# Performance work log

Measured on AMD Instinct MI355X. Metric: run time of the kernel, lower is better.

The kernel has to match this reference:

```python
import jax, jax.numpy as jnp
import numpy as np

B = 32768
H = 320          # pred_hidden
V = 34           # num_classes
BLANK = V - 1    # padding_idx for embedding


def setup_inputs() -> dict:
    key = jax.random.key(0)
    ks = jax.random.split(key, 12)
    s = 0.05
    embed_W = jax.random.normal(ks[0], (V, H), jnp.float32) * s
    embed_W = embed_W.at[BLANK].set(0.0)  # padding_idx row is zeros in torch
    return {
        "x": jax.random.randint(ks[1], (B,), 0, V, jnp.int32),
        "enc_proj_line": jax.random.normal(ks[2], (B, H), jnp.float32),
        "h": jax.random.normal(ks[3], (1, B, H), jnp.float32),
        "c": jax.random.normal(ks[4], (1, B, H), jnp.float32),
        "embed_W": embed_W,
        "W_ih": jax.random.normal(ks[5], (4 * H, H), jnp.float32) * s,
        "W_hh": jax.random.normal(ks[6], (4 * H, H), jnp.float32) * s,
        "b_ih": jax.random.normal(ks[7], (4 * H,), jnp.float32) * s,
        "b_hh": jax.random.normal(ks[8], (4 * H,), jnp.float32) * s,
        "pred_W": jax.random.normal(ks[9], (H, H), jnp.float32) * s,
        "pred_b": jnp.zeros((H,), jnp.float32),
        "joint_W": jax.random.normal(ks[10], (V, H), jnp.float32) * s,
        "joint_b": jnp.zeros((V,), jnp.float32),
    }


def reference(x, enc_proj_line, h, c, embed_W, W_ih, W_hh, b_ih, b_hh,
              pred_W, pred_b, joint_W, joint_b):
    # embedding lookup: [B, H]
    emb = embed_W[x]
    # single-timestep LSTM cell (torch gate order: i, f, g, o)
    gates = emb @ W_ih.T + b_ih + h[0] @ W_hh.T + b_hh  # [B, 4H]
    i, f, g, o = jnp.split(gates, 4, axis=-1)
    i = jax.nn.sigmoid(i)
    f = jax.nn.sigmoid(f)
    g = jnp.tanh(g)
    o = jax.nn.sigmoid(o)
    c_new = f * c[0] + i * g                 # [B, H]
    h_new = o * jnp.tanh(c_new)              # [B, H] == g[0] (lstm output)
    # pred projection + joint
    pred_proj = h_new @ pred_W.T + pred_b    # [B, H]
    joint_out = (enc_proj_line + pred_proj) @ joint_W.T + joint_b  # [B, V]
    dec = jnp.argmax(joint_out, axis=-1)
    return dec, h_new[None], c_new[None]
```

## Files before the change

### kernel.cpp

```cpp
#include <hip/hip_runtime.h>
#include <math.h>

#define NB 32768
#define H 320
#define V 34
#define N4 1280
#define BM 128
#define BN 128
#define BK 32
#define KSTEPS (H / BK)
#define NWG ((NB / BM) * (N4 / BN))

typedef _Float16 f16;
typedef f16 f16x4 __attribute__((ext_vector_type(4)));
typedef f16 f16x8 __attribute__((ext_vector_type(8)));
typedef float f32x4 __attribute__((ext_vector_type(4)));

#define WS_GTP 0
#define WS_JB2 54400
#define WS_B_BYTE 217744
#define BT_COUNT (N4 * H)
#define WS_JP_BYTE 1856144
#define JP_COUNT (48 * 640)
#define WS_AT_BYTE 1979136
#define AT_COUNT (NB * H)

#define JBM 64
#define JBK 32
#define JKSTEPS 20

#define PREP_P4 1280
#define PREP_P2 50
#define PREP_P0 170
#define PREP_P3 120
#define PREP_NWG (PREP_P4 + PREP_P2 + PREP_P0 + PREP_P3 + 1)

__device__ __forceinline__ float sigf(float x) {
    return 1.0f / (1.0f + __expf(-x));
}
__device__ __forceinline__ float tanh_fast(float x) {
    return 1.0f - 2.0f / (1.0f + __expf(2.0f * x));
}

typedef const __attribute__((address_space(1))) unsigned int* gas_t;
typedef __attribute__((address_space(3))) unsigned int* las_t;

__device__ __forceinline__ void split8(const float* e, f16x8& p1, f16x8& p2) {
    #pragma unroll
    for (int j = 0; j < 8; ++j) {
        f16 a = (f16)e[j];
        p1[j] = a;
        p2[j] = (f16)((e[j] - (float)a) * 2048.0f);
    }
}

__global__ void prep(const float* __restrict__ embed_W,
                     const float* __restrict__ W_ih,
                     const float* __restrict__ b_ih,
                     const float* __restrict__ b_hh,
                     const float* __restrict__ pred_W,
                     const float* __restrict__ pred_b,
                     const float* __restrict__ joint_W,
                     const float* __restrict__ joint_b,
                     const float* __restrict__ W_hh,
                     const float* __restrict__ h_in,
                     float* __restrict__ ws) {
    const int bid = blockIdx.x;
    const int t = threadIdx.x;
    if (bid < PREP_P4) {
        int id = bid * 256 + t;
        int ks = id >> 15, m = id & 32767;
        const float* src = h_in + (size_t)m * H + ks * 32;
        f16* at1 = (f16*)((char*)ws + WS_AT_BYTE);
        f16* at2 = at1 + AT_COUNT;
        size_t tbase = ((size_t)(m >> 7) * KSTEPS + ks) * 4096
                       + ((m & 127) >> 4) * 512 + (m & 15) * 8;
        #pragma unroll
        for (int g = 0; g < 4; ++g) {
            float4 v0 = *(const float4*)(src + g * 8);
            float4 v1 = *(const float4*)(src + g * 8 + 4);
            float e[8] = {v0.x, v0.y, v0.z, v0.w, v1.x, v1.y, v1.z, v1.w};
            f16x8 p1, p2;
            split8(e, p1, p2);
            *(f16x8*)(at1 + tbase + g * 128) = p1;
            *(f16x8*)(at2 + tbase + g * 128) = p2;
        }
    } else if (bid < PREP_P4 + PREP_P2) {
        int id = (bid - PREP_P4) * 256 + t;
        int ks = id / 1280, n = id - ks * 1280;
        int orig = (n & 3) * H + (n >> 2);
        const float* src = W_hh + (size_t)orig * H + ks * 32;
        f16* bt1 = (f16*)((char*)ws + WS_B_BYTE);
        f16* bt2 = bt1 + BT_COUNT;
        size_t tbase = ((size_t)(n >> 7) * KSTEPS + ks) * 4096
                       + ((n & 127) >> 4) * 512 + (n & 15) * 8;
        #pragma unroll
        for (int g = 0; g < 4; ++g) {
            float4 v0 = *(const float4*)(src + g * 8);
            float4 v1 = *(const float4*)(src + g * 8 + 4);
            float e[8] = {v0.x, v0.y, v0.z, v0.w, v1.x, v1.y, v1.z, v1.w};
            f16x8 p1, p2;
            split8(e, p1, p2);
            *(f16x8*)(bt1 + tbase + g * 128) = p1;
            *(f16x8*)(bt2 + tbase + g * 128) = p2;
        }
    } else if (bid < PREP_P4 + PREP_P2 + PREP_P0) {
        int id = (bid - PREP_P4 - PREP_P2) * 256 + t;
        int v = id / N4, n = id % N4;
        int orig = (n & 3) * H + (n >> 2);
        float acc = b_ih[orig] + b_hh[orig];
        const float* e = embed_W + (size_t)v * H;
        const float* w = W_ih + (size_t)orig * H;
        for (int k = 0; k < H; k += 4) {
            float4 e4 = *(const float4*)(e + k);
            float4 w4 = *(const float4*)(w + k);
            acc = fmaf(e4.x, w4.x, acc);
            acc = fmaf(e4.y, w4.y, acc);
            acc = fmaf(e4.z, w4.z, acc);
            acc = fmaf(e4.w, w4.w, acc);
        }
        ws[WS_GTP + id] = acc;
    } else if (bid < PREP_P4 + PREP_P2 + PREP_P0 + PREP_P3) {
        int id = (bid - PREP_P4 - PREP_P2 - PREP_P0) * 256 + t;
        int n = id / 640, k = id % 640;
        float wv = 0.0f;
        if (n < V) {
            if (k < H) {
                wv = joint_W[(size_t)n * H + k];
            } else {
                float acc = 0.0f;
                const float* jw = joint_W + (size_t)n * H;
                for (int j = 0; j < H; ++j)
                    acc = fmaf(jw[j], pred_W[(size_t)j * H + (k - H)], acc);
                wv = acc;
            }
        }
        f16 w1 = (f16)wv;
        f16 w2 = (f16)((wv - (float)w1) * 2048.0f);
        int kk = k & 31;
        int off = (k >> 5) * 1536 + (n >> 4) * 512 + (kk >> 3) * 128
                  + (n & 15) * 8 + (kk & 7);
        f16* jp1 = (f16*)((char*)ws + WS_JP_BYTE);
        jp1[off] = w1;
        jp1[JP_COUNT + off] = w2;
    } else {
        if (t < V) {
            float acc = joint_b[t];
            const float* jw = joint_W + (size_t)t * H;
            for (int j = 0; j < H; ++j)
                acc = fmaf(jw[j], pred_b[j], acc);
            ws[WS_JB2 + t] = acc;
        }
    }
}

__launch_bounds__(256, 2)
__global__ void lstm_gemm_fast(const int* __restrict__ x,
                               const float* __restrict__ c_in,
                               const float* __restrict__ ws,
                               float* __restrict__ out) {
    __shared__ __align__(16) char smem[65536];
    const int tid = threadIdx.x, lane = tid & 63, w = tid >> 6;

    int l = (blockIdx.x & 7) * (NWG / 8) + (blockIdx.x >> 3);
    const int mb = l / (N4 / BN);
    const int nb = l % (N4 / BN);
    const int m0 = mb * BM, n0 = nb * BN;

    const f16* At1 = (const f16*)((const char*)ws + WS_AT_BYTE);
    const f16* At2 = At1 + AT_COUNT;
    const f16* Bt1 = (const f16*)((const char*)ws + WS_B_BYTE);
    const f16* Bt2 = Bt1 + BT_COUNT;
    const float* gtp = ws + WS_GTP;
    float* hn_out = out + NB;
    float* cn_out = out + NB + (size_t)NB * H;

    const int asub = (w >> 1) * 4;
    const int bsub = (w & 1) * 4;
    const int lo = lane * 8;

    auto stageB = [&](int ks, int parity) {
        const f16* srcp = (w < 2) ? Bt1 : Bt2;
        const f16* src = srcp + (size_t)(nb * KSTEPS + ks) * 4096 + (w & 1) * 2048;
        char* dst = smem + parity * 16384 + (w >> 1) * 8192 + (w & 1) * 4096;
        #pragma unroll
        for (int i = 0; i < 4; ++i) {
            __builtin_amdgcn_global_load_lds(
                (gas_t)(const void*)(src + i * 512 + lane * 8),
                (las_t)(void*)(dst + i * 1024), 16, 0, 0);
        }
    };

    f32x4 accM[4][4], accC[4][4];
    #pragma unroll
    for (int i = 0; i < 4; ++i)
        #pragma unroll
        for (int j = 0; j < 4; ++j) {
            accM[i][j] = (f32x4){0.f, 0.f, 0.f, 0.f};
            accC[i][j] = (f32x4){0.f, 0.f, 0.f, 0.f};
        }

    f16x8 a1r[2][4], a2r[4], b1[4], b2[4];

    stageB(0, 0);
    __builtin_amdgcn_sched_barrier(0);
    {
        const f16* a1b = At1 + (size_t)(mb * KSTEPS + 0) * 4096;
        #pragma unroll
        for (int mi = 0; mi < 4; ++mi)
            a1r[0][mi] = *(const f16x8*)(a1b + (asub + mi) * 512 + lo);
    }
    asm volatile("s_waitcnt vmcnt(4)" ::: "memory");
    __builtin_amdgcn_sched_barrier(0);
    __builtin_amdgcn_s_barrier();

    #pragma unroll
    for (int t = 0; t < KSTEPS; ++t) {
        const int cb = t & 1;
        {
            const f16* a2b = At2 + (size_t)(mb * KSTEPS + t) * 4096;
            #pragma unroll
            for (int mi = 0; mi < 4; ++mi)
                a2r[mi] = *(const f16x8*)(a2b + (asub + mi) * 512 + lo);
        }
        __builtin_amdgcn_sched_barrier(0);
        if (t < KSTEPS - 1) {
            stageB(t + 1, cb ^ 1);
            __builtin_amdgcn_sched_barrier(0);
            const f16* a1b = At1 + (size_t)(mb * KSTEPS + (t + 1)) * 4096;
            #pragma unroll
            for (int mi = 0; mi < 4; ++mi)
                a1r[cb ^ 1][mi] = *(const f16x8*)(a1b + (asub + mi) * 512 + lo);
            __builtin_amdgcn_sched_barrier(0);
        }

        const f16* B1 = (const f16*)(smem + cb * 16384);
        const f16* B2 = B1 + 4096;

        #pragma unroll
        for (int nj = 0; nj < 4; ++nj)
            b1[nj] = *(const f16x8*)(B1 + (bsub + nj) * 512 + lo);
        __builtin_amdgcn_s_setprio(1);
        #pragma unroll
        for (int mi = 0; mi < 4; ++mi)
            #pragma unroll
            for (int nj = 0; nj < 4; ++nj)
                accM[mi][nj] = __builtin_amdgcn_mfma_f32_16x16x32_f16(
                    a1r[cb][mi], b1[nj], accM[mi][nj], 0, 0, 0);
        __builtin_amdgcn_s_setprio(0);
        #pragma unroll
        for (int nj = 0; nj < 4; ++nj)
            b2[nj] = *(const f16x8*)(B2 + (bsub + nj) * 512 + lo);
        __builtin_amdgcn_s_setprio(1);
        #pragma unroll
        for (int mi = 0; mi < 4; ++mi)
            #pragma unroll
            for (int nj = 0; nj < 4; ++nj)
                accC[mi][nj] = __builtin_amdgcn_mfma_f32_16x16x32_f16(
                    a1r[cb][mi], b2[nj], accC[mi][nj], 0, 0, 0);
        #pragma unroll
        for (int mi = 0; mi < 4; ++mi)
            #pragma unroll
            for (int nj = 0; nj < 4; ++nj)
                accC[mi][nj] = __builtin_amdgcn_mfma_f32_16x16x32_f16(
                    a2r[mi], b1[nj], accC[mi][nj], 0, 0, 0);
        __builtin_amdgcn_s_setprio(0);

        if (t < KSTEPS - 1) {
            asm volatile("s_waitcnt vmcnt(4)" ::: "memory");
            __builtin_amdgcn_sched_barrier(0);
            __builtin_amdgcn_s_barrier();
        } else {
            __syncthreads();
        }
    }

    const int wm = (w >> 1) * 64, wn = (w & 1) * 64;
    float* gates = (float*)smem;
    #pragma unroll
    for (int mi = 0; mi < 4; ++mi)
        #pragma unroll
        for (int nj = 0; nj < 4; ++nj) {
            f32x4 vm = accM[mi][nj];
            f32x4 vc = accC[mi][nj];
            int n = wn + nj * 16 + (lane & 15);
            int mb4 = wm + mi * 16 + (lane >> 4) * 4;
            #pragma unroll
            for (int q = 0; q < 4; ++q) {
                int row = mb4 + q;
                gates[row * 128 + (n ^ ((row & 7) << 2))] =
                    fmaf(vc[q], 1.0f / 2048.0f, vm[q]);
            }
        }
    __syncthreads();

    const int hk0 = n0 >> 2;
    #pragma unroll 4
    for (int it = 0; it < 16; ++it) {
        int idx = it * 256 + tid;
        int ml = idx >> 5, hkl = idx & 31;
        int k0 = (ml & 7) << 2;
        f32x4 g4 = *(const f32x4*)&gates[ml * 128 + ((hkl * 4) ^ k0)];
        int m = m0 + ml;
        int hk = hk0 + hkl;
        int xv = x[m];
        float4 b4 = *(const float4*)(gtp + (size_t)xv * N4 + n0 + hkl * 4);
        float ig = sigf(g4[0] + b4.x);
        float fg = sigf(g4[1] + b4.y);
        float gg = tanh_fast(g4[2] + b4.z);
        float og = sigf(g4[3] + b4.w);
        float cv = c_in[(size_t)m * H + hk];
        float cn = fmaf(fg, cv, ig * gg);
        float hn = og * tanh_fast(cn);
        hn_out[(size_t)m * H + hk] = hn;
        cn_out[(size_t)m * H + hk] = cn;
    }
}

__launch_bounds__(256, 2)
__global__ void joint_argmax(const float* __restrict__ enc,
                             const float* __restrict__ ws,
                             float* __restrict__ out) {
    __shared__ __align__(16) char smem[28672];
    const int tid = threadIdx.x, lane = tid & 63, w = tid >> 6;
    const int m0 = blockIdx.x * JBM;

    const f16* Jp1 = (const f16*)((const char*)ws + WS_JP_BYTE);
    const f16* Jp2 = Jp1 + JP_COUNT;
    const float* hn = out + NB;
    const float* jb2 = ws + WS_JB2;

    f16* base = (f16*)smem;

    f32x4 accM[3], accC[3];
    #pragma unroll
    for (int j = 0; j < 3; ++j) {
        accM[j] = (f32x4){0.f, 0.f, 0.f, 0.f};
        accC[j] = (f32x4){0.f, 0.f, 0.f, 0.f};
    }

    auto stage = [&](int t, f16* A1, f16* A2, f16* B1, f16* B2) {
        const float* srcp = (t < 10) ? enc : hn;
        const int koff = (t % 10) * JBK;
        int row = (tid >> 6) * 16 + (tid & 15);
        int k0 = ((tid & 63) >> 4) * 8;
        const float* sp = srcp + (size_t)(m0 + row) * H + koff + k0;
        float4 v0 = *(const float4*)sp;
        float4 v1 = *(const float4*)(sp + 4);
        float e[8] = {v0.x, v0.y, v0.z, v0.w, v1.x, v1.y, v1.z, v1.w};
        f16x8 p1, p2;
        split8(e, p1, p2);
        *(f16x8*)(A1 + tid * 8) = p1;
        *(f16x8*)(A2 + tid * 8) = p2;
        if (tid < 192) {
            *(int4*)(B1 + tid * 8) = *(const int4*)(Jp1 + t * 1536 + tid * 8);
            *(int4*)(B2 + tid * 8) = *(const int4*)(Jp2 + t * 1536 + tid * 8);
        }
    };

    stage(0, base, base + 2048, base + 4096, base + 5632);
    __syncthreads();

    const int lo = lane * 8;
    int cur = 0;
    for (int t = 0; t < JKSTEPS; ++t) {
        if (t < JKSTEPS - 1) {
            f16* nb_ = base + (cur ^ 1) * 7168;
            stage(t + 1, nb_, nb_ + 2048, nb_ + 4096, nb_ + 5632);
        }
        f16* A1 = base + cur * 7168;
        f16* A2 = A1 + 2048;
        f16* B1 = A1 + 4096;
        f16* B2 = A1 + 5632;

        f16x8 a1 = *(const f16x8*)(A1 + w * 512 + lo);
        f16x8 a2 = *(const f16x8*)(A2 + w * 512 + lo);
        f16x8 b1[3], b2[3];
        #pragma unroll
        for (int nj = 0; nj < 3; ++nj) {
            b1[nj] = *(const f16x8*)(B1 + nj * 512 + lo);
            b2[nj] = *(const f16x8*)(B2 + nj * 512 + lo);
        }
        #pragma unroll
        for (int nj = 0; nj < 3; ++nj) {
            accM[nj] = __builtin_amdgcn_mfma_f32_16x16x32_f16(a1, b1[nj], accM[nj], 0, 0, 0);
            accC[nj] = __builtin_amdgcn_mfma_f32_16x16x32_f16(a1, b2[nj], accC[nj], 0, 0, 0);
            accC[nj] = __builtin_amdgcn_mfma_f32_16x16x32_f16(a2, b1[nj], accC[nj], 0, 0, 0);
        }
        __syncthreads();
        cur ^= 1;
    }

    float* lg = (float*)smem;
    const int wm = w * 16;
    #pragma unroll
    for (int nj = 0; nj < 3; ++nj) {
        int n = nj * 16 + (lane & 15);
        int mr = wm + (lane >> 4) * 4;
        #pragma unroll
        for (int q = 0; q < 4; ++q)
            lg[(mr + q) * 49 + n] = fmaf(accC[nj][q], 1.0f / 2048.0f, accM[nj][q]);
    }
    __syncthreads();

    if (tid < JBM) {
        const float* row = lg + tid * 49;
        float best = row[0] + jb2[0];
        int bi = 0;
        #pragma unroll
        for (int v = 1; v < V; ++v) {
            float t2 = row[v] + jb2[v];
            if (t2 > best) { best = t2; bi = v; }
        }
        out[m0 + tid] = (float)bi;
    }
}

extern "C" void kernel_launch(void* const* d_in, const int* in_sizes, int n_in,
                              void* d_out, int out_size, void* d_ws, size_t ws_size,
                              hipStream_t stream) {
    const int*   x       = (const int*)  d_in[0];
    const float* enc     = (const float*)d_in[1];
    const float* h       = (const float*)d_in[2];
    const float* c       = (const float*)d_in[3];
    const float* embed_W = (const float*)d_in[4];
    const float* W_ih    = (const float*)d_in[5];
    const float* W_hh    = (const float*)d_in[6];
    const float* b_ih    = (const float*)d_in[7];
    const float* b_hh    = (const float*)d_in[8];
    const float* pred_W  = (const float*)d_in[9];
    const float* pred_b  = (const float*)d_in[10];
    const float* joint_W = (const float*)d_in[11];
    const float* joint_b = (const float*)d_in[12];
    float* out = (float*)d_out;
    float* ws  = (float*)d_ws;

    prep<<<PREP_NWG, 256, 0, stream>>>(embed_W, W_ih, b_ih, b_hh,
                                       pred_W, pred_b, joint_W, joint_b,
                                       W_hh, h, ws);
    lstm_gemm_fast<<<NWG, 256, 0, stream>>>(x, c, ws, out);
    joint_argmax<<<NB / JBM, 256, 0, stream>>>(enc, ws, out);
}
```

Baseline: 162.5 us.

## Merge split-precision accumulators and halve LDS to raise GEMM occupancy

Drops the separate correction accumulator by folding the fp16 residual terms into the main accumulator. The A-residual is stored unscaled, and the high A part is multiplied by 2^-11 in registers before it meets the scaled B residual. The gate epilogue now runs in two halves so it fits in 32 KB of shared memory, and launch bounds go from 2 to 3 blocks per CU. The aim is fewer VGPRs and less LDS so more waves can hide latency. The costs are extra fp16 multiplies, an extra barrier round in the epilogue, and possible precision loss from small unscaled residuals underflowing in fp16.

```diff
diff --git a/kernel.cpp b/kernel.cpp
--- a/kernel.cpp
+++ b/kernel.cpp
@@ -51,6 +51,15 @@
         f16 a = (f16)e[j];
         p1[j] = a;
         p2[j] = (f16)((e[j] - (float)a) * 2048.0f);
+    }
+}
+
+__device__ __forceinline__ void split8_res(const float* e, f16x8& p1, f16x8& p2) {
+    #pragma unroll
+    for (int j = 0; j < 8; ++j) {
+        f16 a = (f16)e[j];
+        p1[j] = a;
+        p2[j] = (f16)(e[j] - (float)a);
     }
 }
 
@@ -81,7 +90,7 @@
             float4 v1 = *(const float4*)(src + g * 8 + 4);
             float e[8] = {v0.x, v0.y, v0.z, v0.w, v1.x, v1.y, v1.z, v1.w};
             f16x8 p1, p2;
-            split8(e, p1, p2);
+            split8_res(e, p1, p2);
             *(f16x8*)(at1 + tbase + g * 128) = p1;
             *(f16x8*)(at2 + tbase + g * 128) = p2;
         }
@@ -154,12 +163,12 @@
     }
 }
 
-__launch_bounds__(256, 2)
+__launch_bounds__(256, 3)
 __global__ void lstm_gemm_fast(const int* __restrict__ x,
                                const float* __restrict__ c_in,
                                const float* __restrict__ ws,
                                float* __restrict__ out) {
-    __shared__ __align__(16) char smem[65536];
+    __shared__ __align__(16) char smem[32768];
     const int tid = threadIdx.x, lane = tid & 63, w = tid >> 6;
 
     int l = (blockIdx.x & 7) * (NWG / 8) + (blockIdx.x >> 3);
@@ -191,16 +200,14 @@
         }
     };
 
-    f32x4 accM[4][4], accC[4][4];
+    f32x4 acc[4][4];
     #pragma unroll
     for (int i = 0; i < 4; ++i)
         #pragma unroll
-        for (int j = 0; j < 4; ++j) {
-            accM[i][j] = (f32x4){0.f, 0.f, 0.f, 0.f};
-            accC[i][j] = (f32x4){0.f, 0.f, 0.f, 0.f};
-        }
-
-    f16x8 a1r[2][4], a2r[4], b1[4], b2[4];
+        for (int j = 0; j < 4; ++j)
+            acc[i][j] = (f32x4){0.f, 0.f, 0.f, 0.f};
+
+    f16x8 a1r[2][4], a2rr[4], b1[4], b2[4];
 
     stageB(0, 0);
     __builtin_amdgcn_sched_barrier(0);
@@ -217,11 +224,21 @@
     #pragma unroll
     for (int t = 0; t < KSTEPS; ++t) {
         const int cb = t & 1;
+        const f16* B1 = (const f16*)(smem + cb * 16384);
+        const f16* B2 = B1 + 4096;
+
+        #pragma unroll
+        for (int nj = 0; nj < 4; ++nj)
+            b1[nj] = *(const f16x8*)(B1 + (bsub + nj) * 512 + lo);
+        #pragma unroll
+        for (int nj = 0; nj < 4; ++nj)
+            b2[nj] = *(const f16x8*)(B2 + (bsub + nj) * 512 + lo);
+        __builtin_amdgcn_sched_barrier(0);
         {
             const f16* a2b = At2 + (size_t)(mb * KSTEPS + t) * 4096;
             #pragma unroll
             for (int mi = 0; mi < 4; ++mi)
-                a2r[mi] = *(const f16x8*)(a2b + (asub + mi) * 512 + lo);
+                a2rr[mi] = *(const f16x8*)(a2b + (asub + mi) * 512 + lo);
         }
         __builtin_amdgcn_sched_barrier(0);
         if (t < KSTEPS - 1) {
@@ -234,36 +251,32 @@
             __builtin_amdgcn_sched_barrier(0);
         }
 
-        const f16* B1 = (const f16*)(smem + cb * 16384);
-        const f16* B2 = B1 + 4096;
-
-        #pragma unroll
-        for (int nj = 0; nj < 4; ++nj)
-            b1[nj] = *(const f16x8*)(B1 + (bsub + nj) * 512 + lo);
         __builtin_amdgcn_s_setprio(1);
         #pragma unroll
         for (int mi = 0; mi < 4; ++mi)
             #pragma unroll
             for (int nj = 0; nj < 4; ++nj)
-                accM[mi][nj] = __builtin_amdgcn_mfma_f32_16x16x32_f16(
-                    a1r[cb][mi], b1[nj], accM[mi][nj], 0, 0, 0);
+                acc[mi][nj] = __builtin_amdgcn_mfma_f32_16x16x32_f16(
+                    a1r[cb][mi], b1[nj], acc[mi][nj], 0, 0, 0);
         __builtin_amdgcn_s_setprio(0);
         #pragma unroll
-        for (int nj = 0; nj < 4; ++nj)
-            b2[nj] = *(const f16x8*)(B2 + (bsub + nj) * 512 + lo);
+        for (int mi = 0; mi < 4; ++mi)
+            #pragma unroll
+            for (int j = 0; j < 8; ++j)
+                a1r[cb][mi][j] = a1r[cb][mi][j] * (f16)0.00048828125f;
         __builtin_amdgcn_s_setprio(1);
         #pragma unroll
         for (int mi = 0; mi < 4; ++mi)
             #pragma unroll
             for (int nj = 0; nj < 4; ++nj)
-                accC[mi][nj] = __builtin_amdgcn_mfma_f32_16x16x32_f16(
-                    a1r[cb][mi], b2[nj], accC[mi][nj], 0, 0, 0);
+                acc[mi][nj] = __builtin_amdgcn_mfma_f32_16x16x32_f16(
+                    a1r[cb][mi], b2[nj], acc[mi][nj], 0, 0, 0);
         #pragma unroll
         for (int mi = 0; mi < 4; ++mi)
             #pragma unroll
             for (int nj = 0; nj < 4; ++nj)
-                accC[mi][nj] = __builtin_amdgcn_mfma_f32_16x16x32_f16(
-                    a2r[mi], b1[nj], accC[mi][nj], 0, 0, 0);
+                acc[mi][nj] = __builtin_amdgcn_mfma_f32_16x16x32_f16(
+                    a2rr[mi], b1[nj], acc[mi][nj], 0, 0, 0);
         __builtin_amdgcn_s_setprio(0);
 
         if (t < KSTEPS - 1) {
@@ -275,45 +288,48 @@
         }
     }
 
-    const int wm = (w >> 1) * 64, wn = (w & 1) * 64;
+    const int wn = (w & 1) * 64;
+    const int hk0 = n0 >> 2;
     float* gates = (float*)smem;
     #pragma unroll
-    for (int mi = 0; mi < 4; ++mi)
-        #pragma unroll
-        for (int nj = 0; nj < 4; ++nj) {
-            f32x4 vm = accM[mi][nj];
-            f32x4 vc = accC[mi][nj];
-            int n = wn + nj * 16 + (lane & 15);
-            int mb4 = wm + mi * 16 + (lane >> 4) * 4;
-            #pragma unroll
-            for (int q = 0; q < 4; ++q) {
-                int row = mb4 + q;
-                gates[row * 128 + (n ^ ((row & 7) << 2))] =
-                    fmaf(vc[q], 1.0f / 2048.0f, vm[q]);
-            }
-        }
-    __syncthreads();
-
-    const int hk0 = n0 >> 2;
-    #pragma unroll 4
-    for (int it = 0; it < 16; ++it) {
-        int idx = it * 256 + tid;
-        int ml = idx >> 5, hkl = idx & 31;
-        int k0 = (ml & 7) << 2;
-        f32x4 g4 = *(const f32x4*)&gates[ml * 128 + ((hkl * 4) ^ k0)];
-        int m = m0 + ml;
-        int hk = hk0 + hkl;
-        int xv = x[m];
-        float4 b4 = *(const float4*)(gtp + (size_t)xv * N4 + n0 + hkl * 4);
-        float ig = sigf(g4[0] + b4.x);
-        float fg = sigf(g4[1] + b4.y);
-        float gg = tanh_fast(g4[2] + b4.z);
-        float og = sigf(g4[3] + b4.w);
-        float cv = c_in[(size_t)m * H + hk];
-        float cn = fmaf(fg, cv, ig * gg);
-        float hn = og * tanh_fast(cn);
-        hn_out[(size_t)m * H + hk] = hn;
-        cn_out[(size_t)m * H + hk] = cn;
+    for (int hf = 0; hf < 2; ++hf) {
+        if ((w >> 1) == hf) {
+            #pragma unroll
+            for (int mi = 0; mi < 4; ++mi)
+                #pragma unroll
+                for (int nj = 0; nj < 4; ++nj) {
+                    f32x4 v = acc[mi][nj];
+                    int n = wn + nj * 16 + (lane & 15);
+                    int lr0 = mi * 16 + (lane >> 4) * 4;
+                    #pragma unroll
+                    for (int q = 0; q < 4; ++q) {
+                        int lr = lr0 + q;
+                        gates[lr * 128 + (n ^ ((lr & 7) << 2))] = v[q];
+                    }
+                }
+        }
+        __syncthreads();
+        #pragma unroll 2
+        for (int it = 0; it < 8; ++it) {
+            int idx = it * 256 + tid;
+            int ml = idx >> 5, hkl = idx & 31;
+            int k0 = (ml & 7) << 2;
+            f32x4 g4 = *(const f32x4*)&gates[ml * 128 + ((hkl * 4) ^ k0)];
+            int m = m0 + hf * 64 + ml;
+            int hk = hk0 + hkl;
+            int xv = x[m];
+            float4 b4 = *(const float4*)(gtp + (size_t)xv * N4 + n0 + hkl * 4);
+            float ig = sigf(g4[0] + b4.x);
+            float fg = sigf(g4[1] + b4.y);
+            float gg = tanh_fast(g4[2] + b4.z);
+            float og = sigf(g4[3] + b4.w);
+            float cv = c_in[(size_t)m * H + hk];
+            float cn = fmaf(fg, cv, ig * gg);
+            float hn = og * tanh_fast(cn);
+            hn_out[(size_t)m * H + hk] = hn;
+            cn_out[(size_t)m * H + hk] = cn;
+        }
+        if (hf == 0) __syncthreads();
     }
 }
 
```

Result: no change. 165.3 us (+1.7%).
